# Optimization experiments

Hardware: AMD Instinct MI355X
Metric: run time of the kernel (lower is better)

Reference implementation:

```python
import jax, jax.numpy as jnp
import numpy as np

V = 64                 # |Sigma|
IN_DIM = V + 2         # Sigma + '(' + ')'
OUT_DIM = V + 1        # Sigma + <del>/<end>
H = 512
B = 256
SX = 34                # max proto length 32 + 2 boundaries
SY = 34
BIG_NEG = -1000000000.0


def _one_hot_seq(key, S, batch):
    # '(' at pos 0, L random symbols, ')' at pos L+1, zero padding after
    kl, ks = jax.random.split(key)
    lengths = jax.random.randint(kl, (batch,), 4, S - 1)        # L in [4, S-2]
    syms = jax.random.randint(ks, (S, batch), 0, V)
    pos = jnp.arange(S)[:, None]
    tok = jnp.where(pos == 0, V, jnp.where(pos == lengths[None, :] + 1, V + 1, syms))
    oh = jax.nn.one_hot(tok, IN_DIM, dtype=jnp.float32)
    valid = (pos <= lengths[None, :] + 1).astype(jnp.float32)
    return oh * valid[:, :, None]


def setup_inputs() -> dict:
    key = jax.random.key(0)
    ks = jax.random.split(key, 14)

    def p(k, shape, scale):
        return jax.random.uniform(k, shape, jnp.float32, -scale, scale)

    s = 1.0 / float(np.sqrt(H))
    s2 = 1.0 / float(np.sqrt(2 * H))
    return {
        "sources": _one_hot_seq(ks[0], SX, B),
        "targets": _one_hot_seq(ks[1], SY, B),
        # bidirectional prior LSTM (input IN_DIM -> hidden H, fwd + rev)
        "Wih_f": p(ks[2], (4 * H, IN_DIM), s), "Whh_f": p(ks[3], (4 * H, H), s), "b_f": p(ks[4], (4 * H,), s),
        "Wih_r": p(ks[5], (4 * H, IN_DIM), s), "Whh_r": p(ks[6], (4 * H, H), s), "b_r": p(ks[7], (4 * H,), s),
        # modern LSTM (input IN_DIM -> hidden 2H)
        "Wih_m": p(ks[8], (8 * H, IN_DIM), s2), "Whh_m": p(ks[9], (8 * H, 2 * H), s2), "b_m": p(ks[10], (8 * H,), s2),
        # heads: Linear(2H -> OUT_DIM) + LogSoftmax
        "W_sub": p(ks[11], (OUT_DIM, 2 * H), s2), "b_sub": jnp.zeros((OUT_DIM,), jnp.float32),
        "W_ins": p(ks[12], (OUT_DIM, 2 * H), s2), "b_ins": jnp.zeros((OUT_DIM,), jnp.float32),
    }


def _lstm(x, Wih, Whh, b, hid):
    # torch gate order: i, f, g, o
    bsz = x.shape[1]
    def step(carry, xt):
        h, c = carry
        g = xt @ Wih.T + h @ Whh.T + b
        i, f, gg, o = jnp.split(g, 4, axis=-1)
        c = jax.nn.sigmoid(f) * c + jax.nn.sigmoid(i) * jnp.tanh(gg)
        h = jax.nn.sigmoid(o) * jnp.tanh(c)
        return (h, c), h
    init = (jnp.zeros((bsz, hid), x.dtype), jnp.zeros((bsz, hid), x.dtype))
    _, hs = jax.lax.scan(step, init, x)
    return hs  # [S, B, hid]


def _forward(sources, targets, Wih_f, Whh_f, b_f, Wih_r, Whh_r, b_r,
             Wih_m, Whh_m, b_m, W_sub, b_sub, W_ins, b_ins):
    x_fwd = _lstm(sources, Wih_f, Whh_f, b_f, H)
    x_bwd = _lstm(sources[::-1], Wih_r, Whh_r, b_r, H)[::-1]
    x_emb = jnp.concatenate([x_fwd, x_bwd], axis=-1)   # [SX, B, 2H]
    y_emb = _lstm(targets, Wih_m, Whh_m, b_m, 2 * H)    # [SY, B, 2H]

    # head(x_emb[i] + y_emb[j]) decomposes since Linear is affine
    def pair_logprobs(W, bb):
        lx = jnp.einsum('ibh,oh->ibo', x_emb, W)              # [SX, B, O]
        ly = jnp.einsum('jbh,oh->jbo', y_emb, W) + bb         # [SY, B, O]
        return jax.nn.log_softmax(lx[:, None] + ly[None, :], axis=-1)  # [SX, SY, B, O]

    sub_log = pair_logprobs(W_sub, b_sub)
    ins_log = pair_logprobs(W_ins, b_ins)

    # cell (i, j, b) is computed iff x[i] and y[j] are real (non-padding) one-hots, j <= max_cognat_length
    x_any = sources.sum(-1) > 0                                # [SX, B]
    y_any = targets.sum(-1) > 0                                # [SY, B]
    j_ok = jnp.arange(SY) < SY - 1
    valid = x_any[:, None, :] & (y_any & j_ok[:, None])[None, :, :]   # [SX, SY, B]

    end = jnp.where(valid, ins_log[..., V], BIG_NEG)           # insProbs[V_SIZE]
    dlt = jnp.where(valid, sub_log[..., V], BIG_NEG)           # subProbs[V_SIZE]

    y_next = jnp.pad(targets[1:], ((0, 1), (0, 0), (0, 0)))    # y[j+1], [SY, B, IN_DIM]
    ins_ok = valid & (y_next[..., IN_DIM - 1] == 0)[None]      # not bool(y[j+1, V_SIZE+1])
    ins_val = jnp.einsum('ijbv,jbv->ijb', ins_log[..., :V], y_next[..., :V])
    sub_val = jnp.einsum('ijbv,jbv->ijb', sub_log[..., :V], y_next[..., :V])

    # stacked cached probs: [ins, sub, end, del], each [SX, SY, B]
    return jnp.stack([
        jnp.where(ins_ok, ins_val, BIG_NEG),
        jnp.where(ins_ok, sub_val, BIG_NEG),
        end,
        dlt,
    ])


def reference(sources, targets, Wih_f, Whh_f, b_f, Wih_r, Whh_r, b_r,
              Wih_m, Whh_m, b_m, W_sub, b_sub, W_ins, b_ins):
    return _forward(sources, targets, Wih_f, Whh_f, b_f, Wih_r, Whh_r, b_r,
                    Wih_m, Whh_m, b_m, W_sub, b_sub, W_ins, b_ins)
```

## Files before the change

### kernel.cpp

```cpp
#include <hip/hip_runtime.h>

typedef __attribute__((ext_vector_type(4))) float f32x4;
typedef unsigned char u8;
typedef unsigned long long u64t;

#define BIG_NEG -1000000000.0f

static constexpr int B_  = 256;
static constexpr int SX_ = 34;
static constexpr int SY_ = 34;
static constexpr int IND = 66;
static constexpr int OP_ = 80;

__device__ __forceinline__ f32x4 mfma_fp8(long a, long b, f32x4 c) {
  return __builtin_amdgcn_mfma_f32_16x16x32_fp8_fp8(a, b, c, 0, 0, 0);
}
__device__ __forceinline__ float sigm(float x)  { return 1.0f / (1.0f + __expf(-x)); }
__device__ __forceinline__ float tanhx(float x) { return 2.0f * sigm(2.0f * x) - 1.0f; }
template <bool HI>
__device__ __forceinline__ unsigned pk2(float a, float b, unsigned old) {
  return __builtin_amdgcn_cvt_pk_fp8_f32(a, b, (int)old, HI);
}
__device__ __forceinline__ float rsel(f32x4 a, int j) {
  float lo = (j & 1) ? a[1] : a[0];
  float hi = (j & 1) ? a[3] : a[2];
  return (j & 2) ? hi : lo;
}

__global__ __launch_bounds__(256) void prep_all(
    const float* __restrict__ src, const float* __restrict__ tgt,
    int* __restrict__ tok_x, int* __restrict__ tok_y,
    const float* __restrict__ Wsub, const float* __restrict__ Wins,
    u8* __restrict__ Wcat,
    const float* __restrict__ Wihf, const float* __restrict__ bf,
    const float* __restrict__ Wihr, const float* __restrict__ br,
    const float* __restrict__ Wihm, const float* __restrict__ bm,
    float* __restrict__ Ef, float* __restrict__ Er, float* __restrict__ Em,
    const float* __restrict__ Whf, const float* __restrict__ Whr,
    const float* __restrict__ Whm,
    u8* __restrict__ w8f, u8* __restrict__ w8r, u8* __restrict__ w8m) {
  __shared__ float tile[64 * 67];
  const int blk = blockIdx.x;
  const int tid = threadIdx.x;

  if (blk < 68) {
    int idx = blk * 256 + tid;
    const int half = SX_ * B_;
    const float* base = (idx < half) ? src : tgt;
    int* outp         = (idx < half) ? tok_x : tok_y;
    int k = (idx < half) ? idx : idx - half;
    const float* p = base + (size_t)k * IND;
    int tok = -1;
    for (int v = 0; v < IND; ++v) if (p[v] > 0.5f) tok = v;
    outp[k] = tok;
  } else if (blk < 228) {
    int widx = (blk - 68) * 256 + tid;
    int row = widx >> 8;
    int wc  = widx & 255;
    int srow = row < 80 ? row : row - 80;
    const float* W = row < 80 ? Wsub : Wins;
    float f0 = 0.f, f1 = 0.f, f2 = 0.f, f3 = 0.f;
    if (srow < 65) {
      const float* p = W + (size_t)srow * 1024 + wc * 4;
      f0 = p[0]; f1 = p[1]; f2 = p[2]; f3 = p[3];
    }
    unsigned w = pk2<false>(f0, f1, 0);
    w = pk2<true>(f2, f3, w);
    ((unsigned*)Wcat)[widx] = w;
  } else if (blk < 356) {
    int tb = blk - 228;
    const float* W; const float* bias; float* E; int H4; int n0;
    if (tb < 32)      { W = Wihf; bias = bf; E = Ef; H4 = 2048; n0 = tb * 64; }
    else if (tb < 64) { W = Wihr; bias = br; E = Er; H4 = 2048; n0 = (tb - 32) * 64; }
    else              { W = Wihm; bias = bm; E = Em; H4 = 4096; n0 = (tb - 64) * 64; }
    const float* s2 = W + (size_t)n0 * IND;
    for (int i = tid; i < 64 * IND; i += 256) {
      int n = i / IND, v = i - n * IND;
      tile[n * 67 + v] = s2[i];
    }
    __syncthreads();
    int lane = tid & 63, w2 = tid >> 6;
    float bl = bias[n0 + lane];
    for (int v = w2; v < 67; v += 4) {
      float val = (v < 66 ? tile[lane * 67 + v] : 0.f) + bl;
      E[(size_t)v * H4 + n0 + lane] = val;
    }
  } else {
    const int F4 = 2048 * 512 / 4;
    const int M4 = 4096 * 1024 / 4;
    int i = (blk - 356) * 256 + tid;
    int stride = 3072 * 256;
    for (; i < 2 * F4 + M4; i += stride) {
      const float* s3; unsigned* dst; int k;
      if (i < F4)          { s3 = Whf; dst = (unsigned*)w8f; k = i; }
      else if (i < 2 * F4) { s3 = Whr; dst = (unsigned*)w8r; k = i - F4; }
      else                 { s3 = Whm; dst = (unsigned*)w8m; k = i - 2 * F4; }
      float4 f = ((const float4*)s3)[k];
      unsigned w3 = pk2<false>(f.x, f.y, 0);
      w3 = pk2<true>(f.z, f.w, w3);
      dst[k] = w3;
    }
  }
}


template <int HH, int NS>
__device__ __forceinline__ void run_lstm32(
    const u8* __restrict__ w8, const float* __restrict__ E,
    bool revr, u8* __restrict__ hall, int b0, int h0,
    unsigned* __restrict__ flags, int dom0, int myid,
    u8* __restrict__ alds, u8* __restrict__ hT, const u8* __restrict__ tok_small) {
  const int tid = threadIdx.x;
  const int lane = tid & 63, w = tid >> 6;
  const int lo = lane & 15, q = lane >> 4;
  constexpr int AST = HH + 8;
  constexpr int U8C = HH / 8;
  constexpr int USH = (HH == 1024) ? 7 : 6;
  constexpr int NI  = (32 * U8C) / 256;
  constexpr int NK  = HH / 32;
  const int hh = lo & 7;
  const bool hi = (lo >= 8);
  const int hu_e = h0 + w * 8 + hh;

  long breg0[NK], breg1[NK];
  {
    const u8* brow0 = w8 + (size_t)((lo >> 3) * HH + hu_e) * HH + q * 8;
    const u8* brow1 = w8 + (size_t)((2 + (lo >> 3)) * HH + hu_e) * HH + q * 8;
#pragma unroll
    for (int kk = 0; kk < NK; ++kk) {
      breg0[kk] = *(const long*)(brow0 + kk * 32);
      breg1[kk] = *(const long*)(brow1 + kk * 32);
    }
  }
  float creg[4] = {0.f, 0.f, 0.f, 0.f};

  for (int t = 0; t < 34; ++t) {
    const int tpos = revr ? 33 - t : t;
    const u8* tkp = tok_small + tpos * 32;

    float ev[2][4][2];
#pragma unroll
    for (int mt = 0; mt < 2; ++mt)
#pragma unroll
      for (int rr = 0; rr < 2; ++rr) {
        int r = (hi ? 2 : 0) + rr;
        int v = tkp[mt * 16 + q * 4 + r];
        const float* e = E + (size_t)v * (4 * HH) + hu_e;
        ev[mt][0][rr] = e[0];
        ev[mt][1][rr] = e[HH];
        ev[mt][2][rr] = e[2 * HH];
        ev[mt][3][rr] = e[3 * HH];
      }

    f32x4 acc[2][2];
#pragma unroll
    for (int mt = 0; mt < 2; ++mt) {
      acc[mt][0] = (f32x4){0.f, 0.f, 0.f, 0.f};
      acc[mt][1] = (f32x4){0.f, 0.f, 0.f, 0.f};
    }

    if (t > 0) {
      if (tid < NS) {
        const unsigned tgt = (unsigned)t;
        int spin = 0;
        for (;;) {
          unsigned v = __hip_atomic_load(&flags[(dom0 + tid) * 32],
                                         __ATOMIC_RELAXED, __HIP_MEMORY_SCOPE_AGENT);
          if (__ballot(v < tgt) == 0) break;
          __builtin_amdgcn_s_sleep(1);
          if (++spin > (1 << 17)) break;
        }
      }
      __syncthreads();

      const u8* hsrc = hall + (size_t)t * (256 * HH);
      u64t tmp[NI];
#pragma unroll
      for (int ii = 0; ii < NI; ++ii) {
        int idx = tid + ii * 256;
        tmp[ii] = __hip_atomic_load(
            (const u64t*)(hsrc + (size_t)(b0 + (idx >> USH)) * HH + (idx & (U8C - 1)) * 8),
            __ATOMIC_RELAXED, __HIP_MEMORY_SCOPE_AGENT);
      }
#pragma unroll
      for (int ii = 0; ii < NI; ++ii) {
        int idx = tid + ii * 256;
        *(u64t*)&alds[(idx >> USH) * AST + (idx & (U8C - 1)) * 8] = tmp[ii];
      }
      __syncthreads();

      const u8* a0p = alds + lo * AST + q * 8;
      const u8* a1p = alds + (16 + lo) * AST + q * 8;
#pragma unroll
      for (int kk = 0; kk < NK; ++kk) {
        long a0 = *(const long*)(a0p + kk * 32);
        long a1 = *(const long*)(a1p + kk * 32);
        acc[0][0] = mfma_fp8(a0, breg0[kk], acc[0][0]);
        acc[0][1] = mfma_fp8(a0, breg1[kk], acc[0][1]);
        acc[1][0] = mfma_fp8(a1, breg0[kk], acc[1][0]);
        acc[1][1] = mfma_fp8(a1, breg1[kk], acc[1][1]);
      }
    }

#pragma unroll
    for (int mt = 0; mt < 2; ++mt) {
      f32x4 t0 = acc[mt][0], t1 = acc[mt][1];
      f32x4 p0, p1;
#pragma unroll
      for (int c2 = 0; c2 < 4; ++c2) {
        p0[c2] = __shfl_xor(t0[c2], 8, 64);
        p1[c2] = __shfl_xor(t1[c2], 8, 64);
      }
#pragma unroll
      for (int rr = 0; rr < 2; ++rr) {
        int r = (hi ? 2 : 0) + rr;
        float iv = (hi ? p0[r] : t0[r]) + ev[mt][0][rr];
        float fv = (hi ? t0[r] : p0[r]) + ev[mt][1][rr];
        float gv = (hi ? p1[r] : t1[r]) + ev[mt][2][rr];
        float ov = (hi ? t1[r] : p1[r]) + ev[mt][3][rr];
        int m = mt * 16 + q * 4 + r;
        float cold = creg[mt * 2 + rr];
        float cn = sigm(fv) * cold + sigm(iv) * tanhx(gv);
        float hn = sigm(ov) * tanhx(cn);
        creg[mt * 2 + rr] = cn;
        hT[m * 32 + w * 8 + hh] = (u8)(pk2<false>(hn, hn, 0) & 0xffu);
      }
    }
    __syncthreads();

    {
      int m = tid >> 3, cc = tid & 7;
      unsigned val = *(const unsigned*)&hT[m * 32 + cc * 4];
      u8* hdst = hall + (size_t)(t + 1) * (256 * HH);
      __hip_atomic_store((unsigned*)(hdst + (size_t)(b0 + m) * HH + h0 + cc * 4),
                         val, __ATOMIC_RELAXED, __HIP_MEMORY_SCOPE_AGENT);
    }
    if (t < 33) {
      __asm__ volatile("s_waitcnt vmcnt(0)" ::: "memory");
      __syncthreads();
      if (tid == 0)
        __hip_atomic_store(&flags[(dom0 + myid) * 32], (unsigned)(t + 1),
                           __ATOMIC_RELAXED, __HIP_MEMORY_SCOPE_AGENT);
    }
  }
}

template <int HH, int NS>
__device__ __forceinline__ void run_lstm16(
    const u8* __restrict__ w8, const float* __restrict__ E,
    u8* __restrict__ hall, int b0, int h0,
    unsigned* __restrict__ flags, int dom0, int myid,
    u8* __restrict__ alds, u8* __restrict__ hT, const u8* __restrict__ tok_small) {
  const int tid = threadIdx.x;
  const int lane = tid & 63, w = tid >> 6;
  const int lo = lane & 15, q = lane >> 4;
  constexpr int AST = HH + 8;
  constexpr int U8C = HH / 8;
  constexpr int USH = 7;
  constexpr int NI  = (32 * U8C) / 256;
  constexpr int NK  = HH / 32;
  const int g = lo & 3;
  const int u = lo >> 2;
  const int hu = h0 + w * 4 + u;

  long breg[NK];
  {
    const u8* brow = w8 + (size_t)(g * HH + hu) * HH + q * 8;
#pragma unroll
    for (int kk = 0; kk < NK; ++kk) breg[kk] = *(const long*)(brow + kk * 32);
  }
  float creg[2] = {0.f, 0.f};

  for (int t = 0; t < 34; ++t) {
    const u8* tkp = tok_small + t * 32;

    float ev[2][4];
#pragma unroll
    for (int mt = 0; mt < 2; ++mt) {
      int v = tkp[mt * 16 + q * 4 + g];
      const float* e = E + (size_t)v * (4 * HH) + hu;
      ev[mt][0] = e[0]; ev[mt][1] = e[HH]; ev[mt][2] = e[2 * HH]; ev[mt][3] = e[3 * HH];
    }

    f32x4 acc[2];
    acc[0] = (f32x4){0.f, 0.f, 0.f, 0.f};
    acc[1] = (f32x4){0.f, 0.f, 0.f, 0.f};

    if (t > 0) {
      if (tid < NS) {
        const unsigned tgt = (unsigned)t;
        int spin = 0;
        for (;;) {
          unsigned v = __hip_atomic_load(&flags[(dom0 + tid) * 32],
                                         __ATOMIC_RELAXED, __HIP_MEMORY_SCOPE_AGENT);
          if (__ballot(v < tgt) == 0) break;
          __builtin_amdgcn_s_sleep(1);
          if (++spin > (1 << 17)) break;
        }
      }
      __syncthreads();

      const u8* hsrc = hall + (size_t)t * (256 * HH);
      u64t tmp[NI];
#pragma unroll
      for (int ii = 0; ii < NI; ++ii) {
        int idx = tid + ii * 256;
        tmp[ii] = __hip_atomic_load(
            (const u64t*)(hsrc + (size_t)(b0 + (idx >> USH)) * HH + (idx & (U8C - 1)) * 8),
            __ATOMIC_RELAXED, __HIP_MEMORY_SCOPE_AGENT);
      }
#pragma unroll
      for (int ii = 0; ii < NI; ++ii) {
        int idx = tid + ii * 256;
        *(u64t*)&alds[(idx >> USH) * AST + (idx & (U8C - 1)) * 8] = tmp[ii];
      }
      __syncthreads();

      const u8* a0p = alds + lo * AST + q * 8;
      const u8* a1p = alds + (16 + lo) * AST + q * 8;
#pragma unroll
      for (int kk = 0; kk < NK; ++kk) {
        long a0 = *(const long*)(a0p + kk * 32);
        long a1 = *(const long*)(a1p + kk * 32);
        acc[0] = mfma_fp8(a0, breg[kk], acc[0]);
        acc[1] = mfma_fp8(a1, breg[kk], acc[1]);
      }
    }

#pragma unroll
    for (int mt = 0; mt < 2; ++mt) {
      f32x4 a = acc[mt];
      float own = rsel(a, g);
      float y1  = __shfl_xor(rsel(a, g ^ 1), 1, 64);
      float y2  = __shfl_xor(rsel(a, g ^ 2), 2, 64);
      float y3  = __shfl_xor(rsel(a, g ^ 3), 3, 64);
      float iv = (g == 0) ? own : (g == 1) ? y1 : (g == 2) ? y2 : y3;
      float fv = (g == 0) ? y1 : (g == 1) ? own : (g == 2) ? y3 : y2;
      float gv = (g == 0) ? y2 : (g == 1) ? y3 : (g == 2) ? own : y1;
      float ov = (g == 0) ? y3 : (g == 1) ? y2 : (g == 2) ? y1 : own;
      iv += ev[mt][0]; fv += ev[mt][1]; gv += ev[mt][2]; ov += ev[mt][3];
      int m = mt * 16 + q * 4 + g;
      float cold = creg[mt];
      float cn = sigm(fv) * cold + sigm(iv) * tanhx(gv);
      float hn = sigm(ov) * tanhx(cn);
      creg[mt] = cn;
      hT[m * 16 + w * 4 + u] = (u8)(pk2<false>(hn, hn, 0) & 0xffu);
    }
    __syncthreads();

    if (tid < 128) {
      int m = tid >> 2, cc = tid & 3;
      unsigned val = *(const unsigned*)&hT[m * 16 + cc * 4];
      u8* hdst = hall + (size_t)(t + 1) * (256 * HH);
      __hip_atomic_store((unsigned*)(hdst + (size_t)(b0 + m) * HH + h0 + cc * 4),
                         val, __ATOMIC_RELAXED, __HIP_MEMORY_SCOPE_AGENT);
    }
    if (t < 33) {
      __asm__ volatile("s_waitcnt vmcnt(0)" ::: "memory");
      __syncthreads();
      if (tid == 0)
        __hip_atomic_store(&flags[(dom0 + myid) * 32], (unsigned)(t + 1),
                           __ATOMIC_RELAXED, __HIP_MEMORY_SCOPE_AGENT);
    }
  }
}

__global__ __launch_bounds__(256, 3) void lstm_persist(
    const int* __restrict__ tok_x, const int* __restrict__ tok_y,
    const float* __restrict__ E_f, const u8* __restrict__ w8_f,
    const float* __restrict__ E_r, const u8* __restrict__ w8_r,
    const float* __restrict__ E_m, const u8* __restrict__ w8_m,
    u8* __restrict__ fwd_all, u8* __restrict__ rev_all, u8* __restrict__ y_all,
    unsigned* __restrict__ flags) {
  __shared__ u8 alds[32 * 1032] __attribute__((aligned(16)));
  __shared__ u8 hT[32 * 32] __attribute__((aligned(16)));
  __shared__ u8 tok_small[34 * 32];

  const int b = blockIdx.x;
  int role, c, s;
  if (b < 512)      { role = 2; c = b >> 6; s = b & 63; }
  else if (b < 640) { int l = b - 512; role = 0; c = l >> 4; s = l & 15; }
  else              { int l = b - 640; role = 1; c = l >> 4; s = l & 15; }

  const float* E  = role == 0 ? E_f  : role == 1 ? E_r  : E_m;
  const u8*    w8 = role == 0 ? w8_f : role == 1 ? w8_r : w8_m;
  u8* hall        = role == 0 ? fwd_all : role == 1 ? rev_all : y_all;
  const int* tokg = (role == 2) ? tok_y : tok_x;
  const int b0 = c * 32;
  int dom0, h0;
  if (role == 2)      { dom0 = c * 64;       h0 = s * 16; }
  else if (role == 0) { dom0 = 512 + c * 16; h0 = s * 32; }
  else                { dom0 = 640 + c * 16; h0 = s * 32; }

  for (int i = threadIdx.x; i < 34 * 32; i += 256) {
    int t2 = i >> 5, m = i & 31;
    int tk = tokg[t2 * 256 + b0 + m];
    tok_small[i] = (u8)(tk < 0 ? 66 : tk);
  }
  __syncthreads();

  if (role == 2)
    run_lstm16<1024, 64>(w8, E, hall, b0, h0, flags, dom0, s, alds, hT, tok_small);
  else
    run_lstm32<512, 16>(w8, E, role == 1, hall, b0, h0, flags, dom0, s, alds, hT,
                        tok_small);
}

__global__ __launch_bounds__(256, 1) void head_kernel(
    const u8* __restrict__ fwd_all, const u8* __restrict__ rev_all,
    const u8* __restrict__ y_all, const u8* __restrict__ Wcat,
    const float* __restrict__ b_sub, const float* __restrict__ b_ins,
    float* __restrict__ lx_sub, float* __restrict__ lx_ins,
    float* __restrict__ ly_sub, float* __restrict__ ly_ins) {
  __shared__ u8 wq[160 * 264];
  const int lane = threadIdx.x & 63, wave = threadIdx.x >> 6;
  const int lo = lane & 15, q = lane >> 4;
  int blk = blockIdx.x;
  bool yside = (blk >= 136);
  int mb = yside ? blk - 136 : blk;
  int ij = mb >> 2;
  int bbase = (mb & 3) * 64;

  f32x4 acc[10];
#pragma unroll
  for (int nn = 0; nn < 10; ++nn) acc[nn] = (f32x4){0.f,0.f,0.f,0.f};

  for (int qk = 0; qk < 4; ++qk) {
    long aA[8];
    {
      int row = bbase + wave * 16 + lo;
      const u8* ab;
      if (yside)
        ab = y_all + ((size_t)(ij + 1) * 256 + row) * 1024 + qk * 256 + q * 8;
      else if (qk < 2)
        ab = fwd_all + ((size_t)(ij + 1) * 256 + row) * 512 + qk * 256 + q * 8;
      else
        ab = rev_all + ((size_t)(34 - ij) * 256 + row) * 512 + (qk - 2) * 256 + q * 8;
#pragma unroll
      for (int ki = 0; ki < 8; ++ki) aA[ki] = *(const long*)(ab + ki * 32);
    }

    for (int c8 = threadIdx.x; c8 < 160 * 32; c8 += 256) {
      int row = c8 >> 5, col = (c8 & 31) << 3;
      *(long*)&wq[row * 264 + col] =
          *(const long*)&Wcat[(size_t)row * 1024 + qk * 256 + col];
    }
    __syncthreads();

#pragma unroll
    for (int ki = 0; ki < 8; ++ki) {
#pragma unroll
      for (int nn = 0; nn < 10; ++nn) {
        long bf = *(const long*)&wq[(nn * 16 + lo) * 264 + ki * 32 + q * 8];
        acc[nn] = mfma_fp8(aA[ki], bf, acc[nn]);
      }
    }
    __syncthreads();
  }

#pragma unroll
  for (int nn = 0; nn < 10; ++nn) {
    bool is_sub = (nn < 5);
    int n = (is_sub ? nn : nn - 5) * 16 + lo;
    float bias = 0.0f;
    if (yside && n < 65) bias = is_sub ? b_sub[n] : b_ins[n];
    float* dst = yside ? (is_sub ? ly_sub : ly_ins) : (is_sub ? lx_sub : lx_ins);
#pragma unroll
    for (int r = 0; r < 4; ++r) {
      int b = bbase + wave * 16 + q * 4 + r;
      dst[((size_t)ij * 256 + b) * OP_ + n] = acc[nn][r] + bias;
    }
  }
}

__device__ __forceinline__ void lse_one(const float4* __restrict__ X,
                                        const float* __restrict__ py, int sym,
                                        float& logZ, float& v64, float& vs) {
  float v[68];
  const float4* py4 = (const float4*)py;
#pragma unroll
  for (int q = 0; q < 17; ++q) {
    float4 yb = py4[q];
    v[4 * q + 0] = X[q].x + yb.x;
    v[4 * q + 1] = X[q].y + yb.y;
    v[4 * q + 2] = X[q].z + yb.z;
    v[4 * q + 3] = X[q].w + yb.w;
  }
  float m = v[0];
#pragma unroll
  for (int o = 1; o < 65; ++o) m = fmaxf(m, v[o]);
  float s = 0.0f, vsl = 0.0f;
#pragma unroll
  for (int o = 0; o < 65; ++o) {
    s += __expf(v[o] - m);
    if (o < 64) vsl = (o == sym) ? v[o] : vsl;
  }
  logZ = m + __logf(s);
  v64 = v[64];
  vs = vsl;
}

__global__ __launch_bounds__(256, 1) void pair_kernel(
    const int* __restrict__ tok_x, const int* __restrict__ tok_y,
    const float* __restrict__ lx_sub, const float* __restrict__ lx_ins,
    const float* __restrict__ ly_sub, const float* __restrict__ ly_ins,
    float* __restrict__ out) {
  const int hsel = blockIdx.x >= 136;
  const int rem = hsel ? blockIdx.x - 136 : blockIdx.x;
  const int i = rem >> 2;
  const int bc = rem & 3;
  const int jq = threadIdx.x >> 6;
  const int bl = threadIdx.x & 63;
  const int b = bc * 64 + bl;
  const size_t CH = (size_t)SX_ * SY_ * B_;
  const float* lx = hsel ? lx_ins : lx_sub;
  const float* ly = hsel ? ly_ins : ly_sub;
  float* outA = out + (hsel ? 0 : CH);
  float* outB = out + (hsel ? 2 * CH : 3 * CH);

  float4 X[17];
  {
    const float4* ps = (const float4*)(lx + ((size_t)i * 256 + b) * OP_);
#pragma unroll
    for (int q = 0; q < 17; ++q) X[q] = ps[q];
  }
  int tx = tok_x[i * 256 + b];

  for (int j = jq; j < 34; j += 4) {
    size_t obase = ((size_t)i * SY_ + j) * 256 + b;
    bool dead = (j == SY_ - 1) || (tx < 0);
    if (!dead) {
      int ty = tok_y[j * 256 + b];
      if (ty < 0) dead = true;
    }
    if (dead) {
      outA[obase] = BIG_NEG;
      outB[obase] = BIG_NEG;
      continue;
    }
    int tn = tok_y[(j + 1) * 256 + b];
    bool ins_ok = (tn != 65);
    int sym = (tn >= 0 && tn < 64) ? tn : -1;

    float logZ, v64, vs;
    lse_one(X, ly + ((size_t)j * 256 + b) * OP_, sym, logZ, v64, vs);
    float valB = v64 - logZ;
    float valA = (sym >= 0) ? (vs - logZ) : 0.0f;
    outA[obase] = ins_ok ? valA : BIG_NEG;
    outB[obase] = valB;
  }
}

extern "C" void kernel_launch(void* const* d_in, const int* in_sizes, int n_in,
                              void* d_out, int out_size, void* d_ws, size_t ws_size,
                              hipStream_t stream) {
  const float* sources = (const float*)d_in[0];
  const float* targets = (const float*)d_in[1];
  const float* Wih_f = (const float*)d_in[2];
  const float* Whh_f = (const float*)d_in[3];
  const float* b_f   = (const float*)d_in[4];
  const float* Wih_r = (const float*)d_in[5];
  const float* Whh_r = (const float*)d_in[6];
  const float* b_r   = (const float*)d_in[7];
  const float* Wih_m = (const float*)d_in[8];
  const float* Whh_m = (const float*)d_in[9];
  const float* b_m   = (const float*)d_in[10];
  const float* W_sub = (const float*)d_in[11];
  const float* b_sub = (const float*)d_in[12];
  const float* W_ins = (const float*)d_in[13];
  const float* b_ins = (const float*)d_in[14];
  float* out = (float*)d_out;

  char* w = (char*)d_ws;
  constexpr size_t FLAG_SZ = 768 * 32 * 4;
  constexpr size_t TOK_SZ  = (size_t)SX_ * B_ * 4;
  constexpr size_t WCAT_SZ = (size_t)160 * 1024;
  constexpr size_t W8F_SZ  = (size_t)2048 * 512;
  constexpr size_t W8M_SZ  = (size_t)4096 * 1024;
  constexpr size_t EF_SZ   = (size_t)67 * 2048 * 4;
  constexpr size_t EM_SZ   = (size_t)67 * 4096 * 4;
  constexpr size_t LX_SZ   = (size_t)SX_ * B_ * OP_ * 4;
  constexpr size_t HF_SZ   = (size_t)35 * B_ * 512;
  constexpr size_t HM_SZ   = (size_t)35 * B_ * 1024;

  size_t off = 0;
  unsigned* flags = (unsigned*)(w + off); off += FLAG_SZ;
  int*  tok_x   = (int*)(w + off);  off += TOK_SZ;
  int*  tok_y   = (int*)(w + off);  off += TOK_SZ;
  off = (off + 255) & ~(size_t)255;
  u8*   Wcat    = (u8*)(w + off);   off += WCAT_SZ;
  u8*   w8_f    = (u8*)(w + off);   off += W8F_SZ;
  u8*   w8_r    = (u8*)(w + off);   off += W8F_SZ;
  u8*   w8_m    = (u8*)(w + off);   off += W8M_SZ;
  float* E_f    = (float*)(w + off); off += EF_SZ;
  float* E_r    = (float*)(w + off); off += EF_SZ;
  float* E_m    = (float*)(w + off); off += EM_SZ;
  float* lx_sub = (float*)(w + off); off += LX_SZ;
  float* lx_ins = (float*)(w + off); off += LX_SZ;
  float* ly_sub = (float*)(w + off); off += LX_SZ;
  float* ly_ins = (float*)(w + off); off += LX_SZ;
  u8* fwd_all   = (u8*)(w + off);   off += HF_SZ;
  u8* rev_all   = (u8*)(w + off);   off += HF_SZ;
  u8* y_all     = (u8*)(w + off);   off += HM_SZ;
  (void)ws_size; (void)in_sizes; (void)n_in; (void)out_size;

  (void)hipMemsetAsync(flags, 0, FLAG_SZ, stream);

  prep_all<<<3428, 256, 0, stream>>>(
      sources, targets, tok_x, tok_y,
      W_sub, W_ins, Wcat,
      Wih_f, b_f, Wih_r, b_r, Wih_m, b_m, E_f, E_r, E_m,
      Whh_f, Whh_r, Whh_m, w8_f, w8_r, w8_m);

  lstm_persist<<<768, 256, 0, stream>>>(
      tok_x, tok_y,
      E_f, w8_f,
      E_r, w8_r,
      E_m, w8_m,
      fwd_all, rev_all, y_all, flags);

  head_kernel<<<272, 256, 0, stream>>>(fwd_all, rev_all, y_all, Wcat,
                                       b_sub, b_ins, lx_sub, lx_ins, ly_sub, ly_ins);

  pair_kernel<<<272, 256, 0, stream>>>(tok_x, tok_y, lx_sub, lx_ins,
                                       ly_sub, ly_ins, out);
}
```

Before: 338.2 us.

## Replace flag barriers with poisoned-data polling; split pair kernel finer

```diff
diff --git a/kernel.cpp b/kernel.cpp
--- a/kernel.cpp
+++ b/kernel.cpp
@@ -25,6 +25,10 @@
   float lo = (j & 1) ? a[1] : a[0];
   float hi = (j & 1) ? a[3] : a[2];
   return (j & 2) ? hi : lo;
+}
+__device__ __forceinline__ int word_ok(u64t v) {
+  const unsigned POI = 0x7F7F7F7Fu;
+  return ((unsigned)v != POI) & ((unsigned)(v >> 32) != POI);
 }
 
 __global__ __launch_bounds__(256) void prep_all(
@@ -104,11 +108,10 @@
 }
 
 
-template <int HH, int NS>
+template <int HH>
 __device__ __forceinline__ void run_lstm32(
     const u8* __restrict__ w8, const float* __restrict__ E,
     bool revr, u8* __restrict__ hall, int b0, int h0,
-    unsigned* __restrict__ flags, int dom0, int myid,
     u8* __restrict__ alds, u8* __restrict__ hT, const u8* __restrict__ tok_small) {
   const int tid = threadIdx.x;
   const int lane = tid & 63, w = tid >> 6;
@@ -160,27 +163,42 @@
     }
 
     if (t > 0) {
-      if (tid < NS) {
-        const unsigned tgt = (unsigned)t;
+      const u8* hsrc = hall + (size_t)t * (256 * HH);
+      u64t tmp[NI];
+      {
+        const u64t* p0 = (const u64t*)(hsrc + (size_t)(b0 + (tid >> USH)) * HH +
+                                       (tid & (U8C - 1)) * 8);
         int spin = 0;
         for (;;) {
-          unsigned v = __hip_atomic_load(&flags[(dom0 + tid) * 32],
-                                         __ATOMIC_RELAXED, __HIP_MEMORY_SCOPE_AGENT);
-          if (__ballot(v < tgt) == 0) break;
-          __builtin_amdgcn_s_sleep(1);
-          if (++spin > (1 << 17)) break;
+          tmp[0] = __hip_atomic_load(p0, __ATOMIC_RELAXED, __HIP_MEMORY_SCOPE_AGENT);
+          if (word_ok(tmp[0])) break;
+          if (++spin > (1 << 16)) break;
         }
       }
-      __syncthreads();
-
-      const u8* hsrc = hall + (size_t)t * (256 * HH);
-      u64t tmp[NI];
-#pragma unroll
-      for (int ii = 0; ii < NI; ++ii) {
+      unsigned pend = 0;
+#pragma unroll
+      for (int ii = 1; ii < NI; ++ii) {
         int idx = tid + ii * 256;
         tmp[ii] = __hip_atomic_load(
             (const u64t*)(hsrc + (size_t)(b0 + (idx >> USH)) * HH + (idx & (U8C - 1)) * 8),
             __ATOMIC_RELAXED, __HIP_MEMORY_SCOPE_AGENT);
+        pend |= (word_ok(tmp[ii]) ? 0u : 1u) << ii;
+      }
+      {
+        int spin = 0;
+        while (pend) {
+#pragma unroll
+          for (int ii = 1; ii < NI; ++ii)
+            if (pend & (1u << ii)) {
+              int idx = tid + ii * 256;
+              tmp[ii] = __hip_atomic_load(
+                  (const u64t*)(hsrc + (size_t)(b0 + (idx >> USH)) * HH +
+                                (idx & (U8C - 1)) * 8),
+                  __ATOMIC_RELAXED, __HIP_MEMORY_SCOPE_AGENT);
+              if (word_ok(tmp[ii])) pend &= ~(1u << ii);
+            }
+          if (++spin > (1 << 16)) break;
+        }
       }
 #pragma unroll
       for (int ii = 0; ii < NI; ++ii) {
@@ -235,21 +253,13 @@
       __hip_atomic_store((unsigned*)(hdst + (size_t)(b0 + m) * HH + h0 + cc * 4),
                          val, __ATOMIC_RELAXED, __HIP_MEMORY_SCOPE_AGENT);
     }
-    if (t < 33) {
-      __asm__ volatile("s_waitcnt vmcnt(0)" ::: "memory");
-      __syncthreads();
-      if (tid == 0)
-        __hip_atomic_store(&flags[(dom0 + myid) * 32], (unsigned)(t + 1),
-                           __ATOMIC_RELAXED, __HIP_MEMORY_SCOPE_AGENT);
-    }
-  }
-}
-
-template <int HH, int NS>
+  }
+}
+
+template <int HH>
 __device__ __forceinline__ void run_lstm16(
     const u8* __restrict__ w8, const float* __restrict__ E,
     u8* __restrict__ hall, int b0, int h0,
-    unsigned* __restrict__ flags, int dom0, int myid,
     u8* __restrict__ alds, u8* __restrict__ hT, const u8* __restrict__ tok_small) {
   const int tid = threadIdx.x;
   const int lane = tid & 63, w = tid >> 6;
@@ -287,27 +297,42 @@
     acc[1] = (f32x4){0.f, 0.f, 0.f, 0.f};
 
     if (t > 0) {
-      if (tid < NS) {
-        const unsigned tgt = (unsigned)t;
+      const u8* hsrc = hall + (size_t)t * (256 * HH);
+      u64t tmp[NI];
+      {
+        const u64t* p0 = (const u64t*)(hsrc + (size_t)(b0 + (tid >> USH)) * HH +
+                                       (tid & (U8C - 1)) * 8);
         int spin = 0;
         for (;;) {
-          unsigned v = __hip_atomic_load(&flags[(dom0 + tid) * 32],
-                                         __ATOMIC_RELAXED, __HIP_MEMORY_SCOPE_AGENT);
-          if (__ballot(v < tgt) == 0) break;
-          __builtin_amdgcn_s_sleep(1);
-          if (++spin > (1 << 17)) break;
+          tmp[0] = __hip_atomic_load(p0, __ATOMIC_RELAXED, __HIP_MEMORY_SCOPE_AGENT);
+          if (word_ok(tmp[0])) break;
+          if (++spin > (1 << 16)) break;
         }
       }
-      __syncthreads();
-
-      const u8* hsrc = hall + (size_t)t * (256 * HH);
-      u64t tmp[NI];
-#pragma unroll
-      for (int ii = 0; ii < NI; ++ii) {
+      unsigned pend = 0;
+#pragma unroll
+      for (int ii = 1; ii < NI; ++ii) {
         int idx = tid + ii * 256;
         tmp[ii] = __hip_atomic_load(
             (const u64t*)(hsrc + (size_t)(b0 + (idx >> USH)) * HH + (idx & (U8C - 1)) * 8),
             __ATOMIC_RELAXED, __HIP_MEMORY_SCOPE_AGENT);
+        pend |= (word_ok(tmp[ii]) ? 0u : 1u) << ii;
+      }
+      {
+        int spin = 0;
+        while (pend) {
+#pragma unroll
+          for (int ii = 1; ii < NI; ++ii)
+            if (pend & (1u << ii)) {
+              int idx = tid + ii * 256;
+              tmp[ii] = __hip_atomic_load(
+                  (const u64t*)(hsrc + (size_t)(b0 + (idx >> USH)) * HH +
+                                (idx & (U8C - 1)) * 8),
+                  __ATOMIC_RELAXED, __HIP_MEMORY_SCOPE_AGENT);
+              if (word_ok(tmp[ii])) pend &= ~(1u << ii);
+            }
+          if (++spin > (1 << 16)) break;
+        }
       }
 #pragma unroll
       for (int ii = 0; ii < NI; ++ii) {
@@ -355,13 +380,6 @@
       __hip_atomic_store((unsigned*)(hdst + (size_t)(b0 + m) * HH + h0 + cc * 4),
                          val, __ATOMIC_RELAXED, __HIP_MEMORY_SCOPE_AGENT);
     }
-    if (t < 33) {
-      __asm__ volatile("s_waitcnt vmcnt(0)" ::: "memory");
-      __syncthreads();
-      if (tid == 0)
-        __hip_atomic_store(&flags[(dom0 + myid) * 32], (unsigned)(t + 1),
-                           __ATOMIC_RELAXED, __HIP_MEMORY_SCOPE_AGENT);
-    }
   }
 }
 
@@ -370,8 +388,7 @@
     const float* __restrict__ E_f, const u8* __restrict__ w8_f,
     const float* __restrict__ E_r, const u8* __restrict__ w8_r,
     const float* __restrict__ E_m, const u8* __restrict__ w8_m,
-    u8* __restrict__ fwd_all, u8* __restrict__ rev_all, u8* __restrict__ y_all,
-    unsigned* __restrict__ flags) {
+    u8* __restrict__ fwd_all, u8* __restrict__ rev_all, u8* __restrict__ y_all) {
   __shared__ u8 alds[32 * 1032] __attribute__((aligned(16)));
   __shared__ u8 hT[32 * 32] __attribute__((aligned(16)));
   __shared__ u8 tok_small[34 * 32];
@@ -387,10 +404,7 @@
   u8* hall        = role == 0 ? fwd_all : role == 1 ? rev_all : y_all;
   const int* tokg = (role == 2) ? tok_y : tok_x;
   const int b0 = c * 32;
-  int dom0, h0;
-  if (role == 2)      { dom0 = c * 64;       h0 = s * 16; }
-  else if (role == 0) { dom0 = 512 + c * 16; h0 = s * 32; }
-  else                { dom0 = 640 + c * 16; h0 = s * 32; }
+  const int h0 = (role == 2) ? s * 16 : s * 32;
 
   for (int i = threadIdx.x; i < 34 * 32; i += 256) {
     int t2 = i >> 5, m = i & 31;
@@ -400,10 +414,9 @@
   __syncthreads();
 
   if (role == 2)
-    run_lstm16<1024, 64>(w8, E, hall, b0, h0, flags, dom0, s, alds, hT, tok_small);
+    run_lstm16<1024>(w8, E, hall, b0, h0, alds, hT, tok_small);
   else
-    run_lstm32<512, 16>(w8, E, role == 1, hall, b0, h0, flags, dom0, s, alds, hT,
-                        tok_small);
+    run_lstm32<512>(w8, E, role == 1, hall, b0, h0, alds, hT, tok_small);
 }
 
 __global__ __launch_bounds__(256, 1) void head_kernel(
@@ -473,45 +486,18 @@
   }
 }
 
-__device__ __forceinline__ void lse_one(const float4* __restrict__ X,
-                                        const float* __restrict__ py, int sym,
-                                        float& logZ, float& v64, float& vs) {
-  float v[68];
-  const float4* py4 = (const float4*)py;
-#pragma unroll
-  for (int q = 0; q < 17; ++q) {
-    float4 yb = py4[q];
-    v[4 * q + 0] = X[q].x + yb.x;
-    v[4 * q + 1] = X[q].y + yb.y;
-    v[4 * q + 2] = X[q].z + yb.z;
-    v[4 * q + 3] = X[q].w + yb.w;
-  }
-  float m = v[0];
-#pragma unroll
-  for (int o = 1; o < 65; ++o) m = fmaxf(m, v[o]);
-  float s = 0.0f, vsl = 0.0f;
-#pragma unroll
-  for (int o = 0; o < 65; ++o) {
-    s += __expf(v[o] - m);
-    if (o < 64) vsl = (o == sym) ? v[o] : vsl;
-  }
-  logZ = m + __logf(s);
-  v64 = v[64];
-  vs = vsl;
-}
-
-__global__ __launch_bounds__(256, 1) void pair_kernel(
+__global__ __launch_bounds__(256) void pair_kernel(
     const int* __restrict__ tok_x, const int* __restrict__ tok_y,
     const float* __restrict__ lx_sub, const float* __restrict__ lx_ins,
     const float* __restrict__ ly_sub, const float* __restrict__ ly_ins,
     float* __restrict__ out) {
-  const int hsel = blockIdx.x >= 136;
-  const int rem = hsel ? blockIdx.x - 136 : blockIdx.x;
-  const int i = rem >> 2;
-  const int bc = rem & 3;
-  const int jq = threadIdx.x >> 6;
-  const int bl = threadIdx.x & 63;
-  const int b = bc * 64 + bl;
+  const int hsel = blockIdx.x >= 272;
+  const int rem = hsel ? blockIdx.x - 272 : blockIdx.x;
+  const int i = rem >> 3;
+  const int bc = rem & 7;
+  const int jq = threadIdx.x >> 5;
+  const int bl = threadIdx.x & 31;
+  const int b = bc * 32 + bl;
   const size_t CH = (size_t)SX_ * SY_ * B_;
   const float* lx = hsel ? lx_ins : lx_sub;
   const float* ly = hsel ? ly_ins : ly_sub;
@@ -526,7 +512,7 @@
   }
   int tx = tok_x[i * 256 + b];
 
-  for (int j = jq; j < 34; j += 4) {
+  for (int j = jq; j < 34; j += 8) {
     size_t obase = ((size_t)i * SY_ + j) * 256 + b;
     bool dead = (j == SY_ - 1) || (tx < 0);
     if (!dead) {
@@ -542,8 +528,33 @@
     bool ins_ok = (tn != 65);
     int sym = (tn >= 0 && tn < 64) ? tn : -1;
 
-    float logZ, v64, vs;
-    lse_one(X, ly + ((size_t)j * 256 + b) * OP_, sym, logZ, v64, vs);
+    const float4* py4 = (const float4*)(ly + ((size_t)j * 256 + b) * OP_);
+    float m = -3.0e38f;
+#pragma unroll
+    for (int q = 0; q < 16; ++q) {
+      float4 yb = py4[q];
+      float a0 = X[q].x + yb.x, a1 = X[q].y + yb.y;
+      float a2 = X[q].z + yb.z, a3 = X[q].w + yb.w;
+      m = fmaxf(m, fmaxf(fmaxf(a0, a1), fmaxf(a2, a3)));
+    }
+    float v64 = X[16].x + py4[16].x;
+    m = fmaxf(m, v64);
+    float s = 0.0f, vs = 0.0f;
+#pragma unroll
+    for (int q = 0; q < 16; ++q) {
+      float4 yb = py4[q];
+      float a0 = X[q].x + yb.x, a1 = X[q].y + yb.y;
+      float a2 = X[q].z + yb.z, a3 = X[q].w + yb.w;
+      s += __expf(a0 - m) + __expf(a1 - m) + __expf(a2 - m) + __expf(a3 - m);
+      int o0 = 4 * q;
+      vs = (o0     == sym) ? a0 : vs;
+      vs = (o0 + 1 == sym) ? a1 : vs;
+      vs = (o0 + 2 == sym) ? a2 : vs;
+      vs = (o0 + 3 == sym) ? a3 : vs;
+    }
+    s += __expf(v64 - m);
+    float logZ = m + __logf(s);
+
     float valB = v64 - logZ;
     float valA = (sym >= 0) ? (vs - logZ) : 0.0f;
     outA[obase] = ins_ok ? valA : BIG_NEG;
@@ -572,7 +583,6 @@
   float* out = (float*)d_out;
 
   char* w = (char*)d_ws;
-  constexpr size_t FLAG_SZ = 768 * 32 * 4;
   constexpr size_t TOK_SZ  = (size_t)SX_ * B_ * 4;
   constexpr size_t WCAT_SZ = (size_t)160 * 1024;
   constexpr size_t W8F_SZ  = (size_t)2048 * 512;
@@ -584,7 +594,6 @@
   constexpr size_t HM_SZ   = (size_t)35 * B_ * 1024;
 
   size_t off = 0;
-  unsigned* flags = (unsigned*)(w + off); off += FLAG_SZ;
   int*  tok_x   = (int*)(w + off);  off += TOK_SZ;
   int*  tok_y   = (int*)(w + off);  off += TOK_SZ;
   off = (off + 255) & ~(size_t)255;
@@ -604,7 +613,7 @@
   u8* y_all     = (u8*)(w + off);   off += HM_SZ;
   (void)ws_size; (void)in_sizes; (void)n_in; (void)out_size;
 
-  (void)hipMemsetAsync(flags, 0, FLAG_SZ, stream);
+  (void)hipMemsetAsync(fwd_all, 0x7F, HF_SZ * 2 + HM_SZ, stream);
 
   prep_all<<<3428, 256, 0, stream>>>(
       sources, targets, tok_x, tok_y,
@@ -617,11 +626,11 @@
       E_f, w8_f,
       E_r, w8_r,
       E_m, w8_m,
-      fwd_all, rev_all, y_all, flags);
+      fwd_all, rev_all, y_all);
 
   head_kernel<<<272, 256, 0, stream>>>(fwd_all, rev_all, y_all, Wcat,
                                        b_sub, b_ins, lx_sub, lx_ins, ly_sub, ly_ins);
 
-  pair_kernel<<<272, 256, 0, stream>>>(tok_x, tok_y, lx_sub, lx_ins,
+  pair_kernel<<<544, 256, 0, stream>>>(tok_x, tok_y, lx_sub, lx_ins,
                                        ly_sub, ly_ins, out);
 }
```

New measurement: 524.0 us. +55.0%, slower.

## Replace per-block step flags with sharded per-step atomic counters in persistent LSTM

Applied to the files above, without the earlier changes.

```diff
diff --git a/kernel.cpp b/kernel.cpp
--- a/kernel.cpp
+++ b/kernel.cpp
@@ -25,6 +25,9 @@
   float lo = (j & 1) ? a[1] : a[0];
   float hi = (j & 1) ? a[3] : a[2];
   return (j & 2) ? hi : lo;
+}
+__device__ __forceinline__ int cidx(int dom, int t, int s) {
+  return ((dom * 40 + t) * 8 + s) * 32;
 }
 
 __global__ __launch_bounds__(256) void prep_all(
@@ -104,11 +107,11 @@
 }
 
 
-template <int HH, int NS>
+template <int HH, int NSUB, int TGT>
 __device__ __forceinline__ void run_lstm32(
     const u8* __restrict__ w8, const float* __restrict__ E,
     bool revr, u8* __restrict__ hall, int b0, int h0,
-    unsigned* __restrict__ flags, int dom0, int myid,
+    unsigned* __restrict__ cnt, int dom, int myid,
     u8* __restrict__ alds, u8* __restrict__ hT, const u8* __restrict__ tok_small) {
   const int tid = threadIdx.x;
   const int lane = tid & 63, w = tid >> 6;
@@ -160,13 +163,12 @@
     }
 
     if (t > 0) {
-      if (tid < NS) {
-        const unsigned tgt = (unsigned)t;
+      if (tid < NSUB) {
         int spin = 0;
         for (;;) {
-          unsigned v = __hip_atomic_load(&flags[(dom0 + tid) * 32],
+          unsigned v = __hip_atomic_load(&cnt[cidx(dom, t, tid)],
                                          __ATOMIC_RELAXED, __HIP_MEMORY_SCOPE_AGENT);
-          if (__ballot(v < tgt) == 0) break;
+          if (__ballot(v < (unsigned)TGT) == 0) break;
           __builtin_amdgcn_s_sleep(1);
           if (++spin > (1 << 17)) break;
         }
@@ -228,28 +230,30 @@
     }
     __syncthreads();
 
-    {
-      int m = tid >> 3, cc = tid & 7;
-      unsigned val = *(const unsigned*)&hT[m * 32 + cc * 4];
+    if (w == 3) {
+      int m = lane >> 1, half = lane & 1;
+      const u8* s = &hT[m * 32 + half * 16];
+      u64t v0 = *(const u64t*)(s);
+      u64t v1 = *(const u64t*)(s + 8);
       u8* hdst = hall + (size_t)(t + 1) * (256 * HH);
-      __hip_atomic_store((unsigned*)(hdst + (size_t)(b0 + m) * HH + h0 + cc * 4),
-                         val, __ATOMIC_RELAXED, __HIP_MEMORY_SCOPE_AGENT);
-    }
-    if (t < 33) {
-      __asm__ volatile("s_waitcnt vmcnt(0)" ::: "memory");
-      __syncthreads();
-      if (tid == 0)
-        __hip_atomic_store(&flags[(dom0 + myid) * 32], (unsigned)(t + 1),
-                           __ATOMIC_RELAXED, __HIP_MEMORY_SCOPE_AGENT);
-    }
-  }
-}
-
-template <int HH, int NS>
+      u8* d = hdst + (size_t)(b0 + m) * HH + h0 + half * 16;
+      __hip_atomic_store((u64t*)d, v0, __ATOMIC_RELAXED, __HIP_MEMORY_SCOPE_AGENT);
+      __hip_atomic_store((u64t*)(d + 8), v1, __ATOMIC_RELAXED, __HIP_MEMORY_SCOPE_AGENT);
+      if (t < 33) {
+        __asm__ volatile("s_waitcnt vmcnt(0)" ::: "memory");
+        if (lane == 0)
+          __hip_atomic_fetch_add(&cnt[cidx(dom, t + 1, myid & (NSUB - 1))], 1u,
+                                 __ATOMIC_RELAXED, __HIP_MEMORY_SCOPE_AGENT);
+      }
+    }
+  }
+}
+
+template <int HH, int NSUB, int TGT>
 __device__ __forceinline__ void run_lstm16(
     const u8* __restrict__ w8, const float* __restrict__ E,
     u8* __restrict__ hall, int b0, int h0,
-    unsigned* __restrict__ flags, int dom0, int myid,
+    unsigned* __restrict__ cnt, int dom, int myid,
     u8* __restrict__ alds, u8* __restrict__ hT, const u8* __restrict__ tok_small) {
   const int tid = threadIdx.x;
   const int lane = tid & 63, w = tid >> 6;
@@ -287,13 +291,12 @@
     acc[1] = (f32x4){0.f, 0.f, 0.f, 0.f};
 
     if (t > 0) {
-      if (tid < NS) {
-        const unsigned tgt = (unsigned)t;
+      if (tid < NSUB) {
         int spin = 0;
         for (;;) {
-          unsigned v = __hip_atomic_load(&flags[(dom0 + tid) * 32],
+          unsigned v = __hip_atomic_load(&cnt[cidx(dom, t, tid)],
                                          __ATOMIC_RELAXED, __HIP_MEMORY_SCOPE_AGENT);
-          if (__ballot(v < tgt) == 0) break;
+          if (__ballot(v < (unsigned)TGT) == 0) break;
           __builtin_amdgcn_s_sleep(1);
           if (++spin > (1 << 17)) break;
         }
@@ -348,19 +351,18 @@
     }
     __syncthreads();
 
-    if (tid < 128) {
-      int m = tid >> 2, cc = tid & 3;
-      unsigned val = *(const unsigned*)&hT[m * 16 + cc * 4];
+    if (w == 3) {
+      int m = lane >> 1, half = lane & 1;
+      u64t val = *(const u64t*)&hT[m * 16 + half * 8];
       u8* hdst = hall + (size_t)(t + 1) * (256 * HH);
-      __hip_atomic_store((unsigned*)(hdst + (size_t)(b0 + m) * HH + h0 + cc * 4),
+      __hip_atomic_store((u64t*)(hdst + (size_t)(b0 + m) * HH + h0 + half * 8),
                          val, __ATOMIC_RELAXED, __HIP_MEMORY_SCOPE_AGENT);
-    }
-    if (t < 33) {
-      __asm__ volatile("s_waitcnt vmcnt(0)" ::: "memory");
-      __syncthreads();
-      if (tid == 0)
-        __hip_atomic_store(&flags[(dom0 + myid) * 32], (unsigned)(t + 1),
-                           __ATOMIC_RELAXED, __HIP_MEMORY_SCOPE_AGENT);
+      if (t < 33) {
+        __asm__ volatile("s_waitcnt vmcnt(0)" ::: "memory");
+        if (lane == 0)
+          __hip_atomic_fetch_add(&cnt[cidx(dom, t + 1, myid & (NSUB - 1))], 1u,
+                                 __ATOMIC_RELAXED, __HIP_MEMORY_SCOPE_AGENT);
+      }
     }
   }
 }
@@ -371,7 +373,7 @@
     const float* __restrict__ E_r, const u8* __restrict__ w8_r,
     const float* __restrict__ E_m, const u8* __restrict__ w8_m,
     u8* __restrict__ fwd_all, u8* __restrict__ rev_all, u8* __restrict__ y_all,
-    unsigned* __restrict__ flags) {
+    unsigned* __restrict__ cnt) {
   __shared__ u8 alds[32 * 1032] __attribute__((aligned(16)));
   __shared__ u8 hT[32 * 32] __attribute__((aligned(16)));
   __shared__ u8 tok_small[34 * 32];
@@ -387,10 +389,10 @@
   u8* hall        = role == 0 ? fwd_all : role == 1 ? rev_all : y_all;
   const int* tokg = (role == 2) ? tok_y : tok_x;
   const int b0 = c * 32;
-  int dom0, h0;
-  if (role == 2)      { dom0 = c * 64;       h0 = s * 16; }
-  else if (role == 0) { dom0 = 512 + c * 16; h0 = s * 32; }
-  else                { dom0 = 640 + c * 16; h0 = s * 32; }
+  int dom, h0;
+  if (role == 2)      { dom = c;      h0 = s * 16; }
+  else if (role == 0) { dom = 8 + c;  h0 = s * 32; }
+  else                { dom = 16 + c; h0 = s * 32; }
 
   for (int i = threadIdx.x; i < 34 * 32; i += 256) {
     int t2 = i >> 5, m = i & 31;
@@ -400,10 +402,10 @@
   __syncthreads();
 
   if (role == 2)
-    run_lstm16<1024, 64>(w8, E, hall, b0, h0, flags, dom0, s, alds, hT, tok_small);
+    run_lstm16<1024, 8, 8>(w8, E, hall, b0, h0, cnt, dom, s, alds, hT, tok_small);
   else
-    run_lstm32<512, 16>(w8, E, role == 1, hall, b0, h0, flags, dom0, s, alds, hT,
-                        tok_small);
+    run_lstm32<512, 4, 4>(w8, E, role == 1, hall, b0, h0, cnt, dom, s, alds, hT,
+                          tok_small);
 }
 
 __global__ __launch_bounds__(256, 1) void head_kernel(
@@ -572,7 +574,7 @@
   float* out = (float*)d_out;
 
   char* w = (char*)d_ws;
-  constexpr size_t FLAG_SZ = 768 * 32 * 4;
+  constexpr size_t FLAG_SZ = (size_t)24 * 40 * 8 * 32 * 4;
   constexpr size_t TOK_SZ  = (size_t)SX_ * B_ * 4;
   constexpr size_t WCAT_SZ = (size_t)160 * 1024;
   constexpr size_t W8F_SZ  = (size_t)2048 * 512;
@@ -584,7 +586,7 @@
   constexpr size_t HM_SZ   = (size_t)35 * B_ * 1024;
 
   size_t off = 0;
-  unsigned* flags = (unsigned*)(w + off); off += FLAG_SZ;
+  unsigned* cnt = (unsigned*)(w + off); off += FLAG_SZ;
   int*  tok_x   = (int*)(w + off);  off += TOK_SZ;
   int*  tok_y   = (int*)(w + off);  off += TOK_SZ;
   off = (off + 255) & ~(size_t)255;
@@ -604,7 +606,7 @@
   u8* y_all     = (u8*)(w + off);   off += HM_SZ;
   (void)ws_size; (void)in_sizes; (void)n_in; (void)out_size;
 
-  (void)hipMemsetAsync(flags, 0, FLAG_SZ, stream);
+  (void)hipMemsetAsync(cnt, 0, FLAG_SZ, stream);
 
   prep_all<<<3428, 256, 0, stream>>>(
       sources, targets, tok_x, tok_y,
@@ -617,7 +619,7 @@
       E_f, w8_f,
       E_r, w8_r,
       E_m, w8_m,
-      fwd_all, rev_all, y_all, flags);
+      fwd_all, rev_all, y_all, cnt);
 
   head_kernel<<<272, 256, 0, stream>>>(fwd_all, rev_all, y_all, Wcat,
                                        b_sub, b_ins, lx_sub, lx_ins, ly_sub, ly_ins);
```

Result: slower. 367.6 us (+8.7%).
